# Kernel tuning notes

Measured on AMD Instinct MI355X. Metric: run time of the kernel, lower is better.

The kernel has to match this reference:

```python
import jax, jax.numpy as jnp
import numpy as np
import math

IN_C, OUT_C, K, STYLE_DIM = 512, 512, 3, 512
EPS = 1e-8
SCALE = 1.0 / math.sqrt(IN_C * K * K)


def setup_inputs() -> dict:
    key = jax.random.key(0)
    k1, k2, k3, k4, k5 = jax.random.split(key, 5)
    x = jax.random.normal(k1, (8, IN_C, 64, 64), dtype=jnp.float32)
    style = jax.random.normal(k2, (8, STYLE_DIM), dtype=jnp.float32)
    weight = jax.random.normal(k3, (1, OUT_C, IN_C, K, K), dtype=jnp.float32)
    # nn.Linear(style_dim, in_channels): weight [in_channels, style_dim], bias [in_channels]
    lim = 1.0 / math.sqrt(STYLE_DIM)
    style_w = jax.random.uniform(k4, (IN_C, STYLE_DIM), dtype=jnp.float32, minval=-lim, maxval=lim)
    style_b = jax.random.uniform(k5, (IN_C,), dtype=jnp.float32, minval=-lim, maxval=lim)
    return {"x": x, "style": style, "weight": weight, "style_w": style_w, "style_b": style_b}


def _conv_one(xi, wi):
    # xi: [C,H,W], wi: [O,I,K,K]
    out = jax.lax.conv_general_dilated(
        xi[None], wi, window_strides=(1, 1), padding="SAME",
        dimension_numbers=("NCHW", "OIHW", "NCHW"))
    return out[0]


def reference(x, style, weight, style_w, style_b):
    N = x.shape[0]
    s = style @ style_w.T + style_b                      # [N, C_in]
    w = weight * SCALE                                    # [1,O,I,K,K]
    w = w * s[:, None, :, None, None]                     # [N,O,I,K,K]
    demod = jax.lax.rsqrt(jnp.sum(w * w, axis=(2, 3, 4)) + EPS)  # [N,O]
    w = w * demod[:, :, None, None, None]
    out = jax.vmap(_conv_one)(x, w)                       # [N,O,H,W]
    return out
```

## Files before the change

kernel.cpp:

```cpp
#include <hip/hip_runtime.h>
#include <stdint.h>

typedef unsigned short u16;
typedef __bf16 bf16x8 __attribute__((ext_vector_type(8)));
typedef float f32x4 __attribute__((ext_vector_type(4)));

#define SCALE_F 0.014731391274719742f

#define S_OFF   0u
#define DM_OFF  16384u
#define WT_OFF  32768u
#define XS_OFF  4751360u
#define WS_NEED 40435712u

__device__ __forceinline__ u16 f2bf(float f) {
  union { float f; uint32_t u; } c; c.f = f;
  return (u16)((c.u + 0x7FFFu + ((c.u >> 16) & 1u)) >> 16);
}

__device__ __forceinline__ void gload16(const void* g, void* l) {
  __builtin_amdgcn_global_load_lds(
      (const __attribute__((address_space(1))) uint32_t*)g,
      (__attribute__((address_space(3))) uint32_t*)l, 16, 0, 0);
}

__global__ void k_style(const float* __restrict__ style, const float* __restrict__ sw,
                        const float* __restrict__ sb, float* __restrict__ s) {
  int t = blockIdx.x * 256 + threadIdx.x;
  int n = t >> 9, c = t & 511;
  const float4* wr = (const float4*)(sw + (size_t)c * 512);
  const float4* st = (const float4*)(style + (size_t)n * 512);
  float acc = 0.f;
  #pragma unroll 4
  for (int d = 0; d < 128; ++d) {
    float4 a = st[d], b = wr[d];
    acc += a.x * b.x + a.y * b.y + a.z * b.z + a.w * b.w;
  }
  s[t] = acc + sb[c];
}

__global__ __launch_bounds__(256) void k_wt(
    const float* __restrict__ w, const float* __restrict__ s,
    u16* __restrict__ wt, float* __restrict__ dm) {
  __shared__ float wlds[4608];
  __shared__ float slds[4096];
  __shared__ float red[8][4];
  const uint32_t o = blockIdx.x, t = threadIdx.x;
  const uint32_t lane = t & 63u, wv = t >> 6;
  #pragma unroll
  for (uint32_t c = 0; c < 18u; ++c)
    wlds[c * 256u + t] = w[(size_t)o * 4608u + c * 256u + t] * SCALE_F;
  #pragma unroll
  for (uint32_t c = 0; c < 16u; ++c)
    slds[c * 256u + t] = s[c * 256u + t];
  __syncthreads();
  float part[8] = {0.f, 0.f, 0.f, 0.f, 0.f, 0.f, 0.f, 0.f};
  #pragma unroll
  for (uint32_t hh = 0; hh < 2u; ++hh) {
    uint32_t i = hh * 256u + t;
    float q = 0.f;
    #pragma unroll
    for (uint32_t r = 0; r < 9u; ++r) { float a = wlds[i * 9u + r]; q += a * a; }
    #pragma unroll
    for (uint32_t nn = 0; nn < 8u; ++nn) {
      float sv = slds[nn * 512u + i];
      part[nn] += q * sv * sv;
    }
  }
  #pragma unroll
  for (uint32_t nn = 0; nn < 8u; ++nn) {
    float v = part[nn];
    #pragma unroll
    for (uint32_t off = 32u; off >= 1u; off >>= 1) v += __shfl_down(v, off);
    if (lane == 0u) red[nn][wv] = v;
  }
  __syncthreads();
  if (t < 8u)
    dm[t * 512u + o] = rsqrtf(red[t][0] + red[t][1] + red[t][2] + red[t][3] + 1e-8f);
  #pragma unroll 2
  for (uint32_t c = 0; c < 18u; ++c) {
    uint32_t idx = c * 256u + t;
    uint32_t i = idx & 511u, r = idx >> 9;
    wt[(size_t)o * 4608u + idx] = f2bf(wlds[i * 9u + r]);
  }
}

__global__ void k_border(u16* __restrict__ xs) {
  uint32_t tg = blockIdx.x * 256u + threadIdx.x;
  uint32_t q = tg >> 6;
  uint32_t r = tg & 63u;
  uint32_t n = q / 260u, b = q % 260u;
  uint32_t h, w;
  if (b < 66u)        { h = 0u;  w = b; }
  else if (b < 132u)  { h = 65u; w = b - 66u; }
  else { uint32_t c = b - 132u; h = 1u + (c >> 1); w = (c & 1u) * 65u; }
  uint4 z = {0u, 0u, 0u, 0u};
  *(uint4*)(xs + (((size_t)n * 66u + h) * 66u + w) * 512u + r * 8u) = z;
}

__global__ __launch_bounds__(256) void k_xpose(const float* __restrict__ x,
                                               const float* __restrict__ s,
                                               u16* __restrict__ xs) {
  __shared__ u16 tile[64][512];
  uint32_t b = blockIdx.x, n = b >> 6, hs = b & 63u;
  uint32_t t = threadIdx.x;
  const float* xr = x + ((size_t)n * 512u * 64u + hs) * 64u;
  uint32_t w4 = (t & 15u) * 4u;
  uint32_t ib = (t >> 4) * 8u;
  float sv[4][8];
  #pragma unroll
  for (uint32_t p = 0; p < 4u; ++p)
    #pragma unroll
    for (uint32_t j = 0; j < 8u; ++j)
      sv[p][j] = s[n * 512u + p * 128u + ib + j];
  #pragma unroll
  for (uint32_t p = 0; p < 4u; ++p) {
    uint32_t i0 = p * 128u + ib;
    float4 v[8];
    #pragma unroll
    for (uint32_t j = 0; j < 8u; ++j)
      v[j] = *(const float4*)(xr + (size_t)(i0 + j) * 4096u + w4);
    #pragma unroll
    for (uint32_t k = 0; k < 4u; ++k) {
      union { u16 h[8]; uint4 q; } pk;
      #pragma unroll
      for (uint32_t j = 0; j < 8u; ++j) {
        float f = (k == 0u) ? v[j].x : (k == 1u) ? v[j].y : (k == 2u) ? v[j].z : v[j].w;
        pk.h[j] = f2bf(f * sv[p][j]);
      }
      *(uint4*)&tile[w4 + k][i0] = pk.q;
    }
  }
  __syncthreads();
  u16* orow = xs + (((size_t)n * 66u + hs + 1u) * 66u + 1u) * 512u;
  #pragma unroll
  for (uint32_t p = 0; p < 16u; ++p) {
    uint32_t idx = p * 256u + t;
    uint32_t w = idx >> 6, i8 = (idx & 63u) * 8u;
    *(bf16x8*)(orow + (size_t)w * 512u + i8) = *(const bf16x8*)(&tile[w][i8]);
  }
}

__global__ __launch_bounds__(512, 2) void k_conv8(
    const u16* __restrict__ Wt, const u16* __restrict__ Xs,
    const float* __restrict__ Dm, float* __restrict__ out)
{
  extern __shared__ u16 smem[];
  u16* As = smem;
  u16* Bs = smem + 32768;

  const uint32_t bid = blockIdx.x;
  const uint32_t swz = (bid & 7u) * 32u + (bid >> 3);
  const uint32_t n = swz >> 5, ot = (swz >> 4) & 1u, pt = swz & 15u;

  const uint32_t tid = threadIdx.x;
  const uint32_t wid = tid >> 6, lane = tid & 63u;
  const uint32_t l16 = lane & 15u, lg = lane >> 4;
  const uint32_t wm = wid >> 2, wn = wid & 3u;

  const u16* xsn = Xs + (size_t)n * 66u * 66u * 512u;

  f32x4 acc[8][4];
  f32x4 zero = {0.f, 0.f, 0.f, 0.f};
  #pragma unroll
  for (int m = 0; m < 8; ++m)
    #pragma unroll
    for (int nn = 0; nn < 4; ++nn) acc[m][nn] = zero;

  auto stageA = [&](uint32_t Tt, uint32_t half) {
    if (Tt >= 72u) return;
    const uint32_t buf = Tt & 1u;
    const uint32_t r = Tt >> 3, i0 = (Tt & 7u) << 6;
    const uint32_t kh = r / 3u, kw = r % 3u;
    #pragma unroll
    for (uint32_t j = 0; j < 2u; ++j) {
      const uint32_t sl = tid + j * 512u;
      const uint32_t row = sl >> 3, cl = sl & 7u;
      const uint32_t csrc = cl ^ (row & 7u);
      const uint32_t R = half * 128u + row;
      const uint32_t hp = pt * 4u + (R >> 6) + kh, wp = (R & 63u) + kw;
      gload16(xsn + ((size_t)hp * 66u + wp) * 512u + i0 + csrc * 8u,
              As + buf * 16384u + half * 8192u + (wid * 64u + j * 512u) * 8u);
    }
  };
  auto stageB = [&](uint32_t Tt, uint32_t half) {
    if (Tt >= 72u) return;
    const uint32_t buf = Tt & 1u;
    const uint32_t r = Tt >> 3, i0 = (Tt & 7u) << 6;
    #pragma unroll
    for (uint32_t j = 0; j < 2u; ++j) {
      const uint32_t sl = tid + j * 512u;
      const uint32_t row = sl >> 3, cl = sl & 7u;
      const uint32_t csrc = cl ^ (row & 7u);
      const uint32_t o = ot * 256u + half * 128u + row;
      gload16(Wt + (size_t)o * 4608u + r * 512u + i0 + csrc * 8u,
              Bs + buf * 16384u + half * 8192u + (wid * 64u + j * 512u) * 8u);
    }
  };

  stageA(0u, 0u); stageA(0u, 1u); stageB(0u, 0u); stageB(0u, 1u);
  stageA(1u, 0u); stageA(1u, 1u);
  asm volatile("s_waitcnt vmcnt(4)" ::: "memory");
  __builtin_amdgcn_s_barrier();

  bf16x8 a[8][2], b01[2][2], b23[2][2];

  for (uint32_t T = 0; T < 72u; ++T) {
    const uint32_t buf = T & 1u;
    const u16* Ab = As + buf * 16384u;
    const u16* Bb = Bs + buf * 16384u;

    #pragma unroll
    for (uint32_t m = 0; m < 4u; ++m) {
      const uint32_t row = wm * 128u + m * 16u + l16;
      #pragma unroll
      for (uint32_t k = 0; k < 2u; ++k) {
        const uint32_t c = (k * 4u + lg) ^ (row & 7u);
        a[m][k] = *(const bf16x8*)(Ab + row * 64u + c * 8u);
      }
    }
    #pragma unroll
    for (uint32_t nn = 0; nn < 2u; ++nn) {
      const uint32_t row = wn * 64u + nn * 16u + l16;
      #pragma unroll
      for (uint32_t k = 0; k < 2u; ++k) {
        const uint32_t c = (k * 4u + lg) ^ (row & 7u);
        b01[nn][k] = *(const bf16x8*)(Bb + row * 64u + c * 8u);
      }
    }
    stageB(T + 1u, 0u);
    __builtin_amdgcn_s_barrier();
    asm volatile("s_waitcnt lgkmcnt(0)" ::: "memory");
    __builtin_amdgcn_sched_barrier(0);
    __builtin_amdgcn_s_setprio(1);
    #pragma unroll
    for (uint32_t m = 0; m < 4u; ++m)
      #pragma unroll
      for (uint32_t nn = 0; nn < 2u; ++nn)
        #pragma unroll
        for (uint32_t k = 0; k < 2u; ++k)
          acc[m][nn] = __builtin_amdgcn_mfma_f32_16x16x32_bf16(a[m][k], b01[nn][k], acc[m][nn], 0, 0, 0);
    __builtin_amdgcn_s_setprio(0);
    __builtin_amdgcn_s_barrier();

    #pragma unroll
    for (uint32_t m = 0; m < 4u; ++m) {
      const uint32_t row = wm * 128u + (m + 4u) * 16u + l16;
      #pragma unroll
      for (uint32_t k = 0; k < 2u; ++k) {
        const uint32_t c = (k * 4u + lg) ^ (row & 7u);
        a[m + 4u][k] = *(const bf16x8*)(Ab + row * 64u + c * 8u);
      }
    }
    stageB(T + 1u, 1u);
    __builtin_amdgcn_s_barrier();
    asm volatile("s_waitcnt lgkmcnt(0)" ::: "memory");
    __builtin_amdgcn_sched_barrier(0);
    __builtin_amdgcn_s_setprio(1);
    #pragma unroll
    for (uint32_t m = 0; m < 4u; ++m)
      #pragma unroll
      for (uint32_t nn = 0; nn < 2u; ++nn)
        #pragma unroll
        for (uint32_t k = 0; k < 2u; ++k)
          acc[m + 4u][nn] = __builtin_amdgcn_mfma_f32_16x16x32_bf16(a[m + 4u][k], b01[nn][k], acc[m + 4u][nn], 0, 0, 0);
    __builtin_amdgcn_s_setprio(0);
    __builtin_amdgcn_s_barrier();

    #pragma unroll
    for (uint32_t nn = 0; nn < 2u; ++nn) {
      const uint32_t row = wn * 64u + (nn + 2u) * 16u + l16;
      #pragma unroll
      for (uint32_t k = 0; k < 2u; ++k) {
        const uint32_t c = (k * 4u + lg) ^ (row & 7u);
        b23[nn][k] = *(const bf16x8*)(Bb + row * 64u + c * 8u);
      }
    }
    stageA(T + 2u, 0u);
    __builtin_amdgcn_s_barrier();
    asm volatile("s_waitcnt lgkmcnt(0)" ::: "memory");
    __builtin_amdgcn_sched_barrier(0);
    __builtin_amdgcn_s_setprio(1);
    #pragma unroll
    for (uint32_t m = 0; m < 4u; ++m)
      #pragma unroll
      for (uint32_t nn = 0; nn < 2u; ++nn)
        #pragma unroll
        for (uint32_t k = 0; k < 2u; ++k)
          acc[m][nn + 2u] = __builtin_amdgcn_mfma_f32_16x16x32_bf16(a[m][k], b23[nn][k], acc[m][nn + 2u], 0, 0, 0);
    __builtin_amdgcn_s_setprio(0);
    __builtin_amdgcn_s_barrier();

    stageA(T + 2u, 1u);
    __builtin_amdgcn_s_barrier();
    __builtin_amdgcn_s_setprio(1);
    #pragma unroll
    for (uint32_t m = 0; m < 4u; ++m)
      #pragma unroll
      for (uint32_t nn = 0; nn < 2u; ++nn)
        #pragma unroll
        for (uint32_t k = 0; k < 2u; ++k)
          acc[m + 4u][nn + 2u] = __builtin_amdgcn_mfma_f32_16x16x32_bf16(a[m + 4u][k], b23[nn][k], acc[m + 4u][nn + 2u], 0, 0, 0);
    __builtin_amdgcn_s_setprio(0);
    if (T < 70u) {
      asm volatile("s_waitcnt vmcnt(4)" ::: "memory");
    } else {
      asm volatile("s_waitcnt vmcnt(0)" ::: "memory");
    }
    __builtin_amdgcn_s_barrier();
  }

  float dmv[4];
  #pragma unroll
  for (uint32_t nn = 0; nn < 4u; ++nn)
    dmv[nn] = Dm[n * 512u + ot * 256u + wn * 64u + nn * 16u + l16];
  float* op = out + ((size_t)n * 512u + ot * 256u + wn * 64u) * 4096u + pt * 256u + wm * 128u;
  #pragma unroll
  for (uint32_t m = 0; m < 8u; ++m)
    #pragma unroll
    for (uint32_t nn = 0; nn < 4u; ++nn)
      *(f32x4*)(op + (size_t)(nn * 16u + l16) * 4096u + m * 16u + lg * 4u) = acc[m][nn] * dmv[nn];
}

extern "C" void kernel_launch(void* const* d_in, const int* in_sizes, int n_in,
                              void* d_out, int out_size, void* d_ws, size_t ws_size,
                              hipStream_t stream) {
  const float* x       = (const float*)d_in[0];
  const float* style   = (const float*)d_in[1];
  const float* weight  = (const float*)d_in[2];
  const float* style_w = (const float*)d_in[3];
  const float* style_b = (const float*)d_in[4];
  float* out = (float*)d_out;

  if (ws_size < (size_t)WS_NEED) return;

  char* ws = (char*)d_ws;
  float* s  = (float*)(ws + S_OFF);
  float* dm = (float*)(ws + DM_OFF);
  u16*   wt = (u16*)(ws + WT_OFF);
  u16*   xs = (u16*)(ws + XS_OFF);

  (void)hipFuncSetAttribute((const void*)k_conv8,
                            hipFuncAttributeMaxDynamicSharedMemorySize, 131072);

  hipLaunchKernelGGL(k_style,  dim3(16),   dim3(256), 0, stream, style, style_w, style_b, s);
  hipLaunchKernelGGL(k_wt,     dim3(512),  dim3(256), 0, stream, weight, s, wt, dm);
  hipLaunchKernelGGL(k_border, dim3(520),  dim3(256), 0, stream, xs);
  hipLaunchKernelGGL(k_xpose,  dim3(512),  dim3(256), 0, stream, x, s, xs);
  hipLaunchKernelGGL(k_conv8,  dim3(256),  dim3(512), 131072, stream, wt, xs, dm, out);
}
```

Before: 288.6 us.

## Pre-swizzle weights into MFMA fragment layout and load B directly to registers

The weight prep kernel now writes bf16 weights in a blocked layout that matches per-lane MFMA B fragments. The conv kernel loads B straight from global memory into registers instead of staging it through LDS, which halves shared memory use and removes most per-phase barriers. The input transpose kernel also drops its LDS tile and writes directly to the padded NHWC buffer. The trade-off is more global-load latency exposed on the B operand, uncoalesced-style direct stores in xpose, and B data no longer shared through LDS between waves.

```diff
diff --git a/kernel.cpp b/kernel.cpp
--- a/kernel.cpp
+++ b/kernel.cpp
@@ -41,7 +41,7 @@
 
 __global__ __launch_bounds__(256) void k_wt(
     const float* __restrict__ w, const float* __restrict__ s,
-    u16* __restrict__ wt, float* __restrict__ dm) {
+    u16* __restrict__ wt2, float* __restrict__ dm) {
   __shared__ float wlds[4608];
   __shared__ float slds[4096];
   __shared__ float red[8][4];
@@ -77,11 +77,14 @@
   __syncthreads();
   if (t < 8u)
     dm[t * 512u + o] = rsqrtf(red[t][0] + red[t][1] + red[t][2] + red[t][3] + 1e-8f);
+  const uint32_t ob = o >> 4, ol = o & 15u;
   #pragma unroll 2
   for (uint32_t c = 0; c < 18u; ++c) {
     uint32_t idx = c * 256u + t;
     uint32_t i = idx & 511u, r = idx >> 9;
-    wt[(size_t)o * 4608u + idx] = f2bf(wlds[i * 9u + r]);
+    uint32_t pos = ((ob * 144u + (idx >> 5)) << 9) + (((idx >> 3) & 3u) << 7)
+                 + (ol << 3) + (idx & 7u);
+    wt2[pos] = f2bf(wlds[i * 9u + r]);
   }
 }
 
@@ -101,18 +104,12 @@
 __global__ __launch_bounds__(256) void k_xpose(const float* __restrict__ x,
                                                const float* __restrict__ s,
                                                u16* __restrict__ xs) {
-  __shared__ u16 tile[64][512];
   uint32_t b = blockIdx.x, n = b >> 6, hs = b & 63u;
   uint32_t t = threadIdx.x;
   const float* xr = x + ((size_t)n * 512u * 64u + hs) * 64u;
   uint32_t w4 = (t & 15u) * 4u;
   uint32_t ib = (t >> 4) * 8u;
-  float sv[4][8];
-  #pragma unroll
-  for (uint32_t p = 0; p < 4u; ++p)
-    #pragma unroll
-    for (uint32_t j = 0; j < 8u; ++j)
-      sv[p][j] = s[n * 512u + p * 128u + ib + j];
+  u16* orow = xs + (((size_t)n * 66u + hs + 1u) * 66u + 1u) * 512u;
   #pragma unroll
   for (uint32_t p = 0; p < 4u; ++p) {
     uint32_t i0 = p * 128u + ib;
@@ -120,34 +117,28 @@
     #pragma unroll
     for (uint32_t j = 0; j < 8u; ++j)
       v[j] = *(const float4*)(xr + (size_t)(i0 + j) * 4096u + w4);
+    float sv[8];
+    #pragma unroll
+    for (uint32_t j = 0; j < 8u; ++j) sv[j] = s[n * 512u + i0 + j];
     #pragma unroll
     for (uint32_t k = 0; k < 4u; ++k) {
       union { u16 h[8]; uint4 q; } pk;
       #pragma unroll
       for (uint32_t j = 0; j < 8u; ++j) {
         float f = (k == 0u) ? v[j].x : (k == 1u) ? v[j].y : (k == 2u) ? v[j].z : v[j].w;
-        pk.h[j] = f2bf(f * sv[p][j]);
+        pk.h[j] = f2bf(f * sv[j]);
       }
-      *(uint4*)&tile[w4 + k][i0] = pk.q;
-    }
-  }
-  __syncthreads();
-  u16* orow = xs + (((size_t)n * 66u + hs + 1u) * 66u + 1u) * 512u;
-  #pragma unroll
-  for (uint32_t p = 0; p < 16u; ++p) {
-    uint32_t idx = p * 256u + t;
-    uint32_t w = idx >> 6, i8 = (idx & 63u) * 8u;
-    *(bf16x8*)(orow + (size_t)w * 512u + i8) = *(const bf16x8*)(&tile[w][i8]);
+      *(uint4*)(orow + (size_t)(w4 + k) * 512u + i0) = pk.q;
+    }
   }
 }
 
 __global__ __launch_bounds__(512, 2) void k_conv8(
-    const u16* __restrict__ Wt, const u16* __restrict__ Xs,
+    const u16* __restrict__ Wt2, const u16* __restrict__ Xs,
     const float* __restrict__ Dm, float* __restrict__ out)
 {
   extern __shared__ u16 smem[];
   u16* As = smem;
-  u16* Bs = smem + 32768;
 
   const uint32_t bid = blockIdx.x;
   const uint32_t swz = (bid & 7u) * 32u + (bid >> 3);
@@ -183,33 +174,32 @@
               As + buf * 16384u + half * 8192u + (wid * 64u + j * 512u) * 8u);
     }
   };
-  auto stageB = [&](uint32_t Tt, uint32_t half) {
-    if (Tt >= 72u) return;
-    const uint32_t buf = Tt & 1u;
-    const uint32_t r = Tt >> 3, i0 = (Tt & 7u) << 6;
-    #pragma unroll
-    for (uint32_t j = 0; j < 2u; ++j) {
-      const uint32_t sl = tid + j * 512u;
-      const uint32_t row = sl >> 3, cl = sl & 7u;
-      const uint32_t csrc = cl ^ (row & 7u);
-      const uint32_t o = ot * 256u + half * 128u + row;
-      gload16(Wt + (size_t)o * 4608u + r * 512u + i0 + csrc * 8u,
-              Bs + buf * 16384u + half * 8192u + (wid * 64u + j * 512u) * 8u);
-    }
+
+  auto bload = [&](uint32_t nn, uint32_t kk, uint32_t Tt) -> bf16x8 {
+    const uint32_t ob = ot * 16u + wn * 4u + nn;
+    const uint32_t kc = (Tt >> 3) * 16u + (Tt & 7u) * 2u + kk;
+    return *(const bf16x8*)(Wt2 + (((size_t)(ob * 144u + kc)) << 9) + (lane << 3));
   };
 
-  stageA(0u, 0u); stageA(0u, 1u); stageB(0u, 0u); stageB(0u, 1u);
-  stageA(1u, 0u); stageA(1u, 1u);
-  asm volatile("s_waitcnt vmcnt(4)" ::: "memory");
+  bf16x8 a[8][2], b01[2][2], b23[2][2];
+
+  stageA(0u, 0u); stageA(0u, 1u);
+  #pragma unroll
+  for (uint32_t nn = 0; nn < 2u; ++nn)
+    #pragma unroll
+    for (uint32_t k = 0; k < 2u; ++k) {
+      b01[nn][k] = bload(nn, k, 0u);
+      b23[nn][k] = bload(nn + 2u, k, 0u);
+    }
+  asm volatile("s_waitcnt vmcnt(0)" ::: "memory");
+  __builtin_amdgcn_sched_barrier(0);
   __builtin_amdgcn_s_barrier();
-
-  bf16x8 a[8][2], b01[2][2], b23[2][2];
 
   for (uint32_t T = 0; T < 72u; ++T) {
     const uint32_t buf = T & 1u;
     const u16* Ab = As + buf * 16384u;
-    const u16* Bb = Bs + buf * 16384u;
-
+
+    stageA(T + 1u, 0u);
     #pragma unroll
     for (uint32_t m = 0; m < 4u; ++m) {
       const uint32_t row = wm * 128u + m * 16u + l16;
@@ -219,17 +209,6 @@
         a[m][k] = *(const bf16x8*)(Ab + row * 64u + c * 8u);
       }
     }
-    #pragma unroll
-    for (uint32_t nn = 0; nn < 2u; ++nn) {
-      const uint32_t row = wn * 64u + nn * 16u + l16;
-      #pragma unroll
-      for (uint32_t k = 0; k < 2u; ++k) {
-        const uint32_t c = (k * 4u + lg) ^ (row & 7u);
-        b01[nn][k] = *(const bf16x8*)(Bb + row * 64u + c * 8u);
-      }
-    }
-    stageB(T + 1u, 0u);
-    __builtin_amdgcn_s_barrier();
     asm volatile("s_waitcnt lgkmcnt(0)" ::: "memory");
     __builtin_amdgcn_sched_barrier(0);
     __builtin_amdgcn_s_setprio(1);
@@ -241,8 +220,8 @@
         for (uint32_t k = 0; k < 2u; ++k)
           acc[m][nn] = __builtin_amdgcn_mfma_f32_16x16x32_bf16(a[m][k], b01[nn][k], acc[m][nn], 0, 0, 0);
     __builtin_amdgcn_s_setprio(0);
-    __builtin_amdgcn_s_barrier();
-
+
+    stageA(T + 1u, 1u);
     #pragma unroll
     for (uint32_t m = 0; m < 4u; ++m) {
       const uint32_t row = wm * 128u + (m + 4u) * 16u + l16;
@@ -252,8 +231,6 @@
         a[m + 4u][k] = *(const bf16x8*)(Ab + row * 64u + c * 8u);
       }
     }
-    stageB(T + 1u, 1u);
-    __builtin_amdgcn_s_barrier();
     asm volatile("s_waitcnt lgkmcnt(0)" ::: "memory");
     __builtin_amdgcn_sched_barrier(0);
     __builtin_amdgcn_s_setprio(1);
@@ -265,20 +242,17 @@
         for (uint32_t k = 0; k < 2u; ++k)
           acc[m + 4u][nn] = __builtin_amdgcn_mfma_f32_16x16x32_bf16(a[m + 4u][k], b01[nn][k], acc[m + 4u][nn], 0, 0, 0);
     __builtin_amdgcn_s_setprio(0);
-    __builtin_amdgcn_s_barrier();
-
-    #pragma unroll
-    for (uint32_t nn = 0; nn < 2u; ++nn) {
-      const uint32_t row = wn * 64u + (nn + 2u) * 16u + l16;
-      #pragma unroll
-      for (uint32_t k = 0; k < 2u; ++k) {
-        const uint32_t c = (k * 4u + lg) ^ (row & 7u);
-        b23[nn][k] = *(const bf16x8*)(Bb + row * 64u + c * 8u);
-      }
-    }
-    stageA(T + 2u, 0u);
-    __builtin_amdgcn_s_barrier();
-    asm volatile("s_waitcnt lgkmcnt(0)" ::: "memory");
+
+    if (T < 71u) {
+      #pragma unroll
+      for (uint32_t nn = 0; nn < 2u; ++nn)
+        #pragma unroll
+        for (uint32_t k = 0; k < 2u; ++k)
+          b01[nn][k] = bload(nn, k, T + 1u);
+      asm volatile("s_waitcnt vmcnt(8)" ::: "memory");
+    } else {
+      asm volatile("s_waitcnt vmcnt(0)" ::: "memory");
+    }
     __builtin_amdgcn_sched_barrier(0);
     __builtin_amdgcn_s_setprio(1);
     #pragma unroll
@@ -289,10 +263,7 @@
         for (uint32_t k = 0; k < 2u; ++k)
           acc[m][nn + 2u] = __builtin_amdgcn_mfma_f32_16x16x32_bf16(a[m][k], b23[nn][k], acc[m][nn + 2u], 0, 0, 0);
     __builtin_amdgcn_s_setprio(0);
-    __builtin_amdgcn_s_barrier();
-
-    stageA(T + 2u, 1u);
-    __builtin_amdgcn_s_barrier();
+
     __builtin_amdgcn_s_setprio(1);
     #pragma unroll
     for (uint32_t m = 0; m < 4u; ++m)
@@ -302,11 +273,15 @@
         for (uint32_t k = 0; k < 2u; ++k)
           acc[m + 4u][nn + 2u] = __builtin_amdgcn_mfma_f32_16x16x32_bf16(a[m + 4u][k], b23[nn][k], acc[m + 4u][nn + 2u], 0, 0, 0);
     __builtin_amdgcn_s_setprio(0);
-    if (T < 70u) {
+    if (T < 71u) {
+      #pragma unroll
+      for (uint32_t nn = 0; nn < 2u; ++nn)
+        #pragma unroll
+        for (uint32_t k = 0; k < 2u; ++k)
+          b23[nn][k] = bload(nn + 2u, k, T + 1u);
       asm volatile("s_waitcnt vmcnt(4)" ::: "memory");
-    } else {
-      asm volatile("s_waitcnt vmcnt(0)" ::: "memory");
-    }
+    }
+    __builtin_amdgcn_sched_barrier(0);
     __builtin_amdgcn_s_barrier();
   }
 
@@ -341,11 +316,11 @@
   u16*   xs = (u16*)(ws + XS_OFF);
 
   (void)hipFuncSetAttribute((const void*)k_conv8,
-                            hipFuncAttributeMaxDynamicSharedMemorySize, 131072);
+                            hipFuncAttributeMaxDynamicSharedMemorySize, 65536);
 
   hipLaunchKernelGGL(k_style,  dim3(16),   dim3(256), 0, stream, style, style_w, style_b, s);
   hipLaunchKernelGGL(k_wt,     dim3(512),  dim3(256), 0, stream, weight, s, wt, dm);
   hipLaunchKernelGGL(k_border, dim3(520),  dim3(256), 0, stream, xs);
   hipLaunchKernelGGL(k_xpose,  dim3(512),  dim3(256), 0, stream, x, s, xs);
-  hipLaunchKernelGGL(k_conv8,  dim3(256),  dim3(512), 131072, stream, wt, xs, dm, out);
-}
+  hipLaunchKernelGGL(k_conv8,  dim3(256),  dim3(512), 65536, stream, wt, xs, dm, out);
+}
```

After: 287.3 us. Within noise of the previous version (-0.4%).
